# Kernel tuning notes

Measured on AMD Instinct MI355X. Metric: run time of the kernel, lower is better.

## Reference

```python
import jax, jax.numpy as jnp
import numpy as np

N, K, R = 32768, 4096, 256

def setup_inputs() -> dict:
    key = jax.random.key(0)
    k1, k2, k3 = jax.random.split(key, 3)
    H = jax.random.normal(k1, (N, R), dtype=jnp.float32)
    L = jax.random.normal(k2, (K, R), dtype=jnp.float32)
    W_I = jax.random.normal(k3, (R, R), dtype=jnp.float32)
    return {"H": H, "L": L, "W_I": W_I}

def reference(H, L, W_I):
    # Q = W_I @ L^T : (r, k)
    Q = jnp.einsum('rs,ks->rk', W_I, L)
    # M_I = H @ Q : (n, k)
    M_I = jnp.einsum('nr,rk->nk', H, Q)
    A_I = jax.nn.softmax(M_I, axis=1)
    # C_I = A_I @ L : (n, r)
    C_I = jnp.einsum('nk,kr->nr', A_I, L)
    return (C_I, A_I)
```

## Files before the change

kernel.cpp:

```cpp
#include <hip/hip_runtime.h>
#include <hip/hip_bf16.h>
#include <math.h>
#include <stdint.h>

constexpr int N_ROWS = 32768;
constexpr int K_DIM  = 4096;
constexpr int R_DIM  = 256;
constexpr int KP     = 3 * R_DIM;

typedef __bf16 bf16x8 __attribute__((ext_vector_type(8)));
typedef float  f32x4  __attribute__((ext_vector_type(4)));
typedef unsigned short u16x8 __attribute__((ext_vector_type(8)));
typedef unsigned short u16x4 __attribute__((ext_vector_type(4)));

__device__ __forceinline__ unsigned short f2bf(float x) {
    unsigned u = __float_as_uint(x);
    u += 0x7fffu + ((u >> 16) & 1u);
    return (unsigned short)(u >> 16);
}
__device__ __forceinline__ float bf2f(unsigned short h) {
    return __uint_as_float((unsigned)h << 16);
}

__device__ __forceinline__ void gl2lds16(const void* gptr, void* lptr) {
    __builtin_amdgcn_global_load_lds(
        (const __attribute__((address_space(1))) unsigned int*)gptr,
        (__attribute__((address_space(3))) unsigned int*)lptr,
        16, 0, 0);
}

__global__ __launch_bounds__(256)
void gemm_mfma_nt(const unsigned short* __restrict__ A,
                  const unsigned short* __restrict__ B,
                  float* __restrict__ C, int M, int N, int Kc)
{
    __shared__ __align__(16) unsigned short As[128 * 32];
    __shared__ __align__(16) unsigned short Bs[128 * 32];

    const int tid  = threadIdx.x;
    const int wave = tid >> 6, lane = tid & 63;
    const int wm = wave >> 1, wn = wave & 1;
    const long m0 = (long)blockIdx.y * 128;
    const long n0 = (long)blockIdx.x * 128;

    f32x4 acc[4][4] = {};

    const int srow  = lane >> 2;
    const int skoff = (lane & 3) * 8;
    const int c0 = wave, c1 = wave + 4;
    const int kq = (lane >> 4) * 8;
    const int mr = lane & 15;

    for (int k0 = 0; k0 < Kc; k0 += 32) {
        gl2lds16(A + (m0 + c0 * 16 + srow) * (long)Kc + k0 + skoff, &As[c0 * 512]);
        gl2lds16(A + (m0 + c1 * 16 + srow) * (long)Kc + k0 + skoff, &As[c1 * 512]);
        gl2lds16(B + (n0 + c0 * 16 + srow) * (long)Kc + k0 + skoff, &Bs[c0 * 512]);
        gl2lds16(B + (n0 + c1 * 16 + srow) * (long)Kc + k0 + skoff, &Bs[c1 * 512]);
        __syncthreads();

        bf16x8 af[4], bfr[4];
#pragma unroll
        for (int t = 0; t < 4; ++t) {
            af[t]  = *(const bf16x8*)&As[(wm * 64 + t * 16 + mr) * 32 + kq];
            bfr[t] = *(const bf16x8*)&Bs[(wn * 64 + t * 16 + mr) * 32 + kq];
        }
#pragma unroll
        for (int i = 0; i < 4; ++i)
#pragma unroll
            for (int j = 0; j < 4; ++j)
                acc[i][j] = __builtin_amdgcn_mfma_f32_16x16x32_bf16(
                    af[i], bfr[j], acc[i][j], 0, 0, 0);
        __syncthreads();
    }

    const int col = lane & 15, rquad = (lane >> 4) * 4;
#pragma unroll
    for (int i = 0; i < 4; ++i) {
        const long mrow = m0 + wm * 64 + i * 16 + rquad;
#pragma unroll
        for (int j = 0; j < 4; ++j) {
            float* p = C + mrow * (long)N + n0 + wn * 64 + j * 16 + col;
#pragma unroll
            for (int r = 0; r < 4; ++r) p[(long)r * N] = acc[i][j][r];
        }
    }
}

__global__ __launch_bounds__(256)
void k1_ap(const float* __restrict__ A, const float* __restrict__ B,
           unsigned short* __restrict__ Ap)
{
    __shared__ __align__(16) float Asl[16][132];
    __shared__ __align__(16) float Bsl[16][132];
    const int tid = threadIdx.x;
    const int tx = tid & 15, ty = tid >> 4;
    const long m0 = (long)blockIdx.x * 128;
    const long n0 = (long)blockIdx.y * 128;
    const int Kc = R_DIM, N = R_DIM;

    float acc[8][8];
#pragma unroll
    for (int i = 0; i < 8; ++i)
#pragma unroll
        for (int j = 0; j < 8; ++j) acc[i][j] = 0.f;

    for (int k0 = 0; k0 < Kc; k0 += 16) {
#pragma unroll
        for (int q = 0; q < 2; ++q) {
            int fi = tid + 256 * q, row = fi >> 2, col = (fi & 3) * 4;
            float4 v = *(const float4*)(A + (m0 + row) * (long)Kc + k0 + col);
            Asl[col + 0][row] = v.x; Asl[col + 1][row] = v.y;
            Asl[col + 2][row] = v.z; Asl[col + 3][row] = v.w;
        }
#pragma unroll
        for (int q = 0; q < 2; ++q) {
            int fi = tid + 256 * q, row = fi >> 5, col = (fi & 31) * 4;
            float4 v = *(const float4*)(B + (k0 + row) * (long)N + n0 + col);
            *(float4*)&Bsl[row][col] = v;
        }
        __syncthreads();
#pragma unroll
        for (int kk = 0; kk < 16; ++kk) {
            float a[8], b[8];
            *(float4*)&a[0] = *(const float4*)&Asl[kk][ty * 8];
            *(float4*)&a[4] = *(const float4*)&Asl[kk][ty * 8 + 4];
            *(float4*)&b[0] = *(const float4*)&Bsl[kk][tx * 8];
            *(float4*)&b[4] = *(const float4*)&Bsl[kk][tx * 8 + 4];
#pragma unroll
            for (int i = 0; i < 8; ++i)
#pragma unroll
                for (int j = 0; j < 8; ++j)
                    acc[i][j] = fmaf(a[i], b[j], acc[i][j]);
        }
        __syncthreads();
    }
#pragma unroll
    for (int i = 0; i < 8; ++i) {
        const long row = m0 + ty * 8 + i;
        u16x8 hi8, lo8;
#pragma unroll
        for (int j = 0; j < 8; ++j) {
            const unsigned short h = f2bf(acc[i][j]);
            hi8[j] = h;
            lo8[j] = f2bf(acc[i][j] - bf2f(h));
        }
        unsigned short* p = Ap + row * KP + n0 + tx * 8;
        *(u16x8*)(p)              = hi8;
        *(u16x8*)(p + R_DIM)      = hi8;
        *(u16x8*)(p + 2 * R_DIM)  = lo8;
    }
}

__global__ __launch_bounds__(256)
void fused_saw(float* __restrict__ Mio, const unsigned short* __restrict__ LT,
               float* __restrict__ C)
{
    __shared__ __align__(16) unsigned short As[32 * 32];
    __shared__ __align__(16) unsigned short Bs[256 * 32];
    __shared__ float sm[32][8];
    __shared__ float ss[32][8];

    const int tid = threadIdx.x, wave = tid >> 6, lane = tid & 63;
    const long m0 = (long)blockIdx.x * 32;

    const int arow = tid >> 3;
    const int acol = (tid & 7) * 4;
    float* Mrow = Mio + (m0 + arow) * (long)K_DIM;

    {
        float m = -3.4e38f, s = 0.f;
        const float* rp = Mrow + acol;
#pragma unroll 4
        for (int q = 0; q < 128; ++q) {
            float4 v = *(const float4*)(rp + 32 * q);
            float m4 = fmaxf(fmaxf(v.x, v.y), fmaxf(v.z, v.w));
            if (m4 > m) { s *= __expf(m - m4); m = m4; }
            s += __expf(v.x - m) + __expf(v.y - m)
               + __expf(v.z - m) + __expf(v.w - m);
        }
        sm[arow][tid & 7] = m;
        ss[arow][tid & 7] = s;
    }
    __syncthreads();
    float rm, ri;
    {
        float m = sm[arow][0];
#pragma unroll
        for (int t = 1; t < 8; ++t) m = fmaxf(m, sm[arow][t]);
        float S = 0.f;
#pragma unroll
        for (int t = 0; t < 8; ++t) S += ss[arow][t] * __expf(sm[arow][t] - m);
        rm = m; ri = 1.f / S;
    }
    __syncthreads();

    const int srow = lane >> 2, skoff = (lane & 3) * 8;
    const int kq = (lane >> 4) * 8, mr = lane & 15;

    f32x4 acc[2][4] = {};

    for (int k0 = 0; k0 < K_DIM; k0 += 32) {
#pragma unroll
        for (int c4 = 0; c4 < 4; ++c4) {
            const int c = wave * 4 + c4;
            gl2lds16(LT + (c * 16 + srow) * (long)K_DIM + k0 + skoff, &Bs[c * 512]);
        }
        float4 v = *(const float4*)(Mrow + k0 + acol);
        float4 a;
        a.x = __expf(v.x - rm) * ri;
        a.y = __expf(v.y - rm) * ri;
        a.z = __expf(v.z - rm) * ri;
        a.w = __expf(v.w - rm) * ri;
        *(float4*)(Mrow + k0 + acol) = a;
        u16x4 u;
        u[0] = f2bf(a.x); u[1] = f2bf(a.y); u[2] = f2bf(a.z); u[3] = f2bf(a.w);
        *(u16x4*)&As[arow * 32 + acol] = u;
        __syncthreads();

        bf16x8 af[2], bfr[4];
        af[0] = *(const bf16x8*)&As[(mr) * 32 + kq];
        af[1] = *(const bf16x8*)&As[(16 + mr) * 32 + kq];
#pragma unroll
        for (int j = 0; j < 4; ++j)
            bfr[j] = *(const bf16x8*)&Bs[(wave * 64 + j * 16 + mr) * 32 + kq];
#pragma unroll
        for (int i = 0; i < 2; ++i)
#pragma unroll
            for (int j = 0; j < 4; ++j)
                acc[i][j] = __builtin_amdgcn_mfma_f32_16x16x32_bf16(
                    af[i], bfr[j], acc[i][j], 0, 0, 0);
        __syncthreads();
    }

    const int col = lane & 15, rq = (lane >> 4) * 4;
#pragma unroll
    for (int i = 0; i < 2; ++i)
#pragma unroll
        for (int j = 0; j < 4; ++j)
#pragma unroll
            for (int r = 0; r < 4; ++r)
                C[(m0 + i * 16 + rq + r) * (long)R_DIM + wave * 64 + j * 16 + col]
                    = acc[i][j][r];
}

__global__ __launch_bounds__(256)
void prep_B(const float* __restrict__ L, unsigned short* __restrict__ Bp)
{
    const long i = (long)blockIdx.x * 256 + threadIdx.x;
    const long k = i >> 8; const int r = (int)(i & 255);
    const float x = L[i];
    const unsigned short hi = f2bf(x);
    const unsigned short lo = f2bf(x - bf2f(hi));
    unsigned short* row = Bp + k * KP;
    row[r] = hi; row[R_DIM + r] = lo; row[2 * R_DIM + r] = hi;
}

__global__ __launch_bounds__(256)
void prep_LT(const float* __restrict__ L, unsigned short* __restrict__ LT)
{
    const long i = (long)blockIdx.x * 256 + threadIdx.x;
    const long r = i >> 12; const long k = i & 4095;
    LT[r * K_DIM + k] = f2bf(L[k * R_DIM + r]);
}

__global__ __launch_bounds__(256)
void prep_A(const float* __restrict__ P, unsigned short* __restrict__ Ap)
{
    const long i = (long)blockIdx.x * 256 + threadIdx.x;
    const long n = i >> 8; const int r = (int)(i & 255);
    const float x = P[i];
    const unsigned short hi = f2bf(x);
    const unsigned short lo = f2bf(x - bf2f(hi));
    unsigned short* row = Ap + n * KP;
    row[r] = hi; row[R_DIM + r] = hi; row[2 * R_DIM + r] = lo;
}

__global__ __launch_bounds__(256)
void gemm_mfma_a32(const float* __restrict__ A,
                   const unsigned short* __restrict__ B,
                   float* __restrict__ C, int M, int N, int Kc)
{
    __shared__ __align__(16) unsigned short As[128 * 32];
    __shared__ __align__(16) unsigned short Bs[128 * 32];

    const int tid  = threadIdx.x;
    const int wave = tid >> 6, lane = tid & 63;
    const int wm = wave >> 1, wn = wave & 1;
    const long m0 = (long)blockIdx.y * 128;
    const long n0 = (long)blockIdx.x * 128;

    f32x4 acc[4][4] = {};
    const int srow  = lane >> 2, skoff = (lane & 3) * 8;
    const int c0 = wave, c1 = wave + 4;
    const int kq = (lane >> 4) * 8, mr = lane & 15;
    const int arow = tid >> 1, ahalf = (tid & 1) * 16;

    for (int k0 = 0; k0 < Kc; k0 += 32) {
        gl2lds16(B + (n0 + c0 * 16 + srow) * (long)Kc + k0 + skoff, &Bs[c0 * 512]);
        gl2lds16(B + (n0 + c1 * 16 + srow) * (long)Kc + k0 + skoff, &Bs[c1 * 512]);
        {
            const float* g = A + (m0 + arow) * (long)Kc + k0 + ahalf;
            float4 v0 = *(const float4*)(g + 0);
            float4 v1 = *(const float4*)(g + 4);
            float4 v2 = *(const float4*)(g + 8);
            float4 v3 = *(const float4*)(g + 12);
            u16x8 u0, u1;
            u0[0] = f2bf(v0.x); u0[1] = f2bf(v0.y); u0[2] = f2bf(v0.z); u0[3] = f2bf(v0.w);
            u0[4] = f2bf(v1.x); u0[5] = f2bf(v1.y); u0[6] = f2bf(v1.z); u0[7] = f2bf(v1.w);
            u1[0] = f2bf(v2.x); u1[1] = f2bf(v2.y); u1[2] = f2bf(v2.z); u1[3] = f2bf(v2.w);
            u1[4] = f2bf(v3.x); u1[5] = f2bf(v3.y); u1[6] = f2bf(v3.z); u1[7] = f2bf(v3.w);
            *(u16x8*)&As[arow * 32 + ahalf + 0] = u0;
            *(u16x8*)&As[arow * 32 + ahalf + 8] = u1;
        }
        __syncthreads();
        bf16x8 af[4], bfr[4];
#pragma unroll
        for (int t = 0; t < 4; ++t) {
            af[t]  = *(const bf16x8*)&As[(wm * 64 + t * 16 + mr) * 32 + kq];
            bfr[t] = *(const bf16x8*)&Bs[(wn * 64 + t * 16 + mr) * 32 + kq];
        }
#pragma unroll
        for (int i = 0; i < 4; ++i)
#pragma unroll
            for (int j = 0; j < 4; ++j)
                acc[i][j] = __builtin_amdgcn_mfma_f32_16x16x32_bf16(
                    af[i], bfr[j], acc[i][j], 0, 0, 0);
        __syncthreads();
    }
    const int col = lane & 15, rquad = (lane >> 4) * 4;
#pragma unroll
    for (int i = 0; i < 4; ++i) {
        const long mrow = m0 + wm * 64 + i * 16 + rquad;
#pragma unroll
        for (int j = 0; j < 4; ++j) {
            float* p = C + mrow * (long)N + n0 + wn * 64 + j * 16 + col;
#pragma unroll
            for (int r = 0; r < 4; ++r) p[(long)r * N] = acc[i][j][r];
        }
    }
}

template<bool BT>
__global__ __launch_bounds__(256)
void gemm128(const float* __restrict__ A, const float* __restrict__ B,
             float* __restrict__ C, int M, int N, int Kc)
{
    __shared__ __align__(16) float Asl[16][132];
    __shared__ __align__(16) float Bsl[16][132];
    const int tid = threadIdx.x;
    const int tx = tid & 15, ty = tid >> 4;
    const long m0 = (long)blockIdx.x * 128;
    const long n0 = (long)blockIdx.y * 128;
    float acc[8][8];
#pragma unroll
    for (int i = 0; i < 8; ++i)
#pragma unroll
        for (int j = 0; j < 8; ++j) acc[i][j] = 0.f;
    for (int k0 = 0; k0 < Kc; k0 += 16) {
#pragma unroll
        for (int q = 0; q < 2; ++q) {
            int fi = tid + 256 * q, row = fi >> 2, col = (fi & 3) * 4;
            float4 v = *(const float4*)(A + (m0 + row) * (long)Kc + k0 + col);
            Asl[col + 0][row] = v.x; Asl[col + 1][row] = v.y;
            Asl[col + 2][row] = v.z; Asl[col + 3][row] = v.w;
        }
        if (BT) {
#pragma unroll
            for (int q = 0; q < 2; ++q) {
                int fi = tid + 256 * q, row = fi >> 2, col = (fi & 3) * 4;
                float4 v = *(const float4*)(B + (n0 + row) * (long)Kc + k0 + col);
                Bsl[col + 0][row] = v.x; Bsl[col + 1][row] = v.y;
                Bsl[col + 2][row] = v.z; Bsl[col + 3][row] = v.w;
            }
        } else {
#pragma unroll
            for (int q = 0; q < 2; ++q) {
                int fi = tid + 256 * q, row = fi >> 5, col = (fi & 31) * 4;
                float4 v = *(const float4*)(B + (k0 + row) * (long)N + n0 + col);
                *(float4*)&Bsl[row][col] = v;
            }
        }
        __syncthreads();
#pragma unroll
        for (int kk = 0; kk < 16; ++kk) {
            float a[8], b[8];
            *(float4*)&a[0] = *(const float4*)&Asl[kk][ty * 8];
            *(float4*)&a[4] = *(const float4*)&Asl[kk][ty * 8 + 4];
            *(float4*)&b[0] = *(const float4*)&Bsl[kk][tx * 8];
            *(float4*)&b[4] = *(const float4*)&Bsl[kk][tx * 8 + 4];
#pragma unroll
            for (int i = 0; i < 8; ++i)
#pragma unroll
                for (int j = 0; j < 8; ++j)
                    acc[i][j] = fmaf(a[i], b[j], acc[i][j]);
        }
        __syncthreads();
    }
#pragma unroll
    for (int i = 0; i < 8; ++i) {
        float* p = C + (m0 + ty * 8 + i) * (long)N + n0 + tx * 8;
        *(float4*)p       = make_float4(acc[i][0], acc[i][1], acc[i][2], acc[i][3]);
        *(float4*)(p + 4) = make_float4(acc[i][4], acc[i][5], acc[i][6], acc[i][7]);
    }
}

__global__ __launch_bounds__(256)
void softmax_rows(float* __restrict__ Mio)
{
    const long n  = blockIdx.x;
    float* row    = Mio + n * (long)K_DIM;
    const int tid = threadIdx.x;
    float4 v[4];
    float lmax = -3.4e38f;
#pragma unroll
    for (int q = 0; q < 4; ++q) {
        v[q] = ((const float4*)row)[tid + 256 * q];
        lmax = fmaxf(lmax, fmaxf(fmaxf(v[q].x, v[q].y), fmaxf(v[q].z, v[q].w)));
    }
    __shared__ float redmax[4], redsum[4];
#pragma unroll
    for (int off = 32; off > 0; off >>= 1)
        lmax = fmaxf(lmax, __shfl_xor(lmax, off));
    if ((tid & 63) == 0) redmax[tid >> 6] = lmax;
    __syncthreads();
    const float gmax = fmaxf(fmaxf(redmax[0], redmax[1]), fmaxf(redmax[2], redmax[3]));
    float lsum = 0.f;
#pragma unroll
    for (int q = 0; q < 4; ++q) {
        v[q].x = __expf(v[q].x - gmax); v[q].y = __expf(v[q].y - gmax);
        v[q].z = __expf(v[q].z - gmax); v[q].w = __expf(v[q].w - gmax);
        lsum += v[q].x + v[q].y + v[q].z + v[q].w;
    }
#pragma unroll
    for (int off = 32; off > 0; off >>= 1)
        lsum += __shfl_xor(lsum, off);
    if ((tid & 63) == 0) redsum[tid >> 6] = lsum;
    __syncthreads();
    const float inv = 1.f / (redsum[0] + redsum[1] + redsum[2] + redsum[3]);
#pragma unroll
    for (int q = 0; q < 4; ++q) {
        v[q].x *= inv; v[q].y *= inv; v[q].z *= inv; v[q].w *= inv;
        ((float4*)row)[tid + 256 * q] = v[q];
    }
}

extern "C" void kernel_launch(void* const* d_in, const int* in_sizes, int n_in,
                              void* d_out, int out_size, void* d_ws, size_t ws_size,
                              hipStream_t stream)
{
    const float* H  = (const float*)d_in[0];
    const float* L  = (const float*)d_in[1];
    const float* Wi = (const float*)d_in[2];

    float* Cout = (float*)d_out;
    float* Aout = (float*)d_out + (size_t)N_ROWS * R_DIM;

    const size_t szAp = (size_t)N_ROWS * KP * 2;
    const size_t szBp = (size_t)K_DIM * KP * 2;
    const size_t szLT = (size_t)R_DIM * K_DIM * 2;

    if (ws_size >= szAp + szBp + szLT) {
        unsigned short* Ap = (unsigned short*)d_ws;
        unsigned short* Bp = (unsigned short*)((char*)d_ws + szAp);
        unsigned short* LT = (unsigned short*)((char*)d_ws + szAp + szBp);

        k1_ap<<<dim3(N_ROWS / 128, R_DIM / 128), 256, 0, stream>>>(H, Wi, Ap);
        prep_B<<<dim3((K_DIM * R_DIM) / 256), 256, 0, stream>>>(L, Bp);
        prep_LT<<<dim3((R_DIM * K_DIM) / 256), 256, 0, stream>>>(L, LT);
        gemm_mfma_nt<<<dim3(K_DIM / 128, N_ROWS / 128), 256, 0, stream>>>(
            Ap, Bp, Aout, N_ROWS, K_DIM, KP);
        fused_saw<<<dim3(N_ROWS / 32), 256, 0, stream>>>(Aout, LT, Cout);
    } else {
        gemm128<false><<<dim3(N_ROWS / 128, R_DIM / 128), 256, 0, stream>>>(
            H, Wi, Cout, N_ROWS, R_DIM, R_DIM);
        gemm128<true><<<dim3(N_ROWS / 128, K_DIM / 128), 256, 0, stream>>>(
            Cout, L, Aout, N_ROWS, K_DIM, R_DIM);
        softmax_rows<<<dim3(N_ROWS), 256, 0, stream>>>(Aout);
        gemm128<false><<<dim3(N_ROWS / 128, R_DIM / 128), 256, 0, stream>>>(
            Aout, L, Cout, N_ROWS, R_DIM, K_DIM);
    }
}
```

Baseline: 1.345 ms.

## Double-buffer B tiles and build softmax A fragments in registers in fused kernel

```diff
diff --git a/kernel.cpp b/kernel.cpp
--- a/kernel.cpp
+++ b/kernel.cpp
@@ -152,24 +152,22 @@
 }
 
 __global__ __launch_bounds__(256)
-void fused_saw(float* __restrict__ Mio, const unsigned short* __restrict__ LT,
-               float* __restrict__ C)
-{
-    __shared__ __align__(16) unsigned short As[32 * 32];
-    __shared__ __align__(16) unsigned short Bs[256 * 32];
+void fused_saw2(float* __restrict__ Mio, const unsigned short* __restrict__ LT,
+                float* __restrict__ C)
+{
+    __shared__ __align__(16) unsigned short Bs[2][256 * 32];
     __shared__ float sm[32][8];
     __shared__ float ss[32][8];
+    __shared__ float rowm[32];
+    __shared__ float rowiv[32];
 
     const int tid = threadIdx.x, wave = tid >> 6, lane = tid & 63;
     const long m0 = (long)blockIdx.x * 32;
 
-    const int arow = tid >> 3;
-    const int acol = (tid & 7) * 4;
-    float* Mrow = Mio + (m0 + arow) * (long)K_DIM;
-
+    const int arow = tid >> 3, acol = (tid & 7) * 4;
     {
+        const float* rp = Mio + (m0 + arow) * (long)K_DIM + acol;
         float m = -3.4e38f, s = 0.f;
-        const float* rp = Mrow + acol;
 #pragma unroll 4
         for (int q = 0; q < 128; ++q) {
             float4 v = *(const float4*)(rp + 32 * q);
@@ -182,54 +180,93 @@
         ss[arow][tid & 7] = s;
     }
     __syncthreads();
-    float rm, ri;
-    {
+    if ((tid & 7) == 0) {
         float m = sm[arow][0];
 #pragma unroll
         for (int t = 1; t < 8; ++t) m = fmaxf(m, sm[arow][t]);
         float S = 0.f;
 #pragma unroll
         for (int t = 0; t < 8; ++t) S += ss[arow][t] * __expf(sm[arow][t] - m);
-        rm = m; ri = 1.f / S;
-    }
-    __syncthreads();
+        rowm[arow] = m;
+        rowiv[arow] = 1.f / S;
+    }
+    __syncthreads();
+
+    const int fr = lane & 15;
+    const int kq = (lane >> 4) * 8;
+    const float rm0 = rowm[fr],      ri0 = rowiv[fr];
+    const float rm1 = rowm[fr + 16], ri1 = rowiv[fr + 16];
 
     const int srow = lane >> 2, skoff = (lane & 3) * 8;
-    const int kq = (lane >> 4) * 8, mr = lane & 15;
-
-    f32x4 acc[2][4] = {};
-
-    for (int k0 = 0; k0 < K_DIM; k0 += 32) {
+
+    float* R0 = Mio + (m0 + fr) * (long)K_DIM + kq;
+    float* R1 = R0 + 16 * (long)K_DIM;
+
+    auto stageB = [&](int buf, int k0) {
 #pragma unroll
         for (int c4 = 0; c4 < 4; ++c4) {
             const int c = wave * 4 + c4;
-            gl2lds16(LT + (c * 16 + srow) * (long)K_DIM + k0 + skoff, &Bs[c * 512]);
-        }
-        float4 v = *(const float4*)(Mrow + k0 + acol);
-        float4 a;
-        a.x = __expf(v.x - rm) * ri;
-        a.y = __expf(v.y - rm) * ri;
-        a.z = __expf(v.z - rm) * ri;
-        a.w = __expf(v.w - rm) * ri;
-        *(float4*)(Mrow + k0 + acol) = a;
-        u16x4 u;
-        u[0] = f2bf(a.x); u[1] = f2bf(a.y); u[2] = f2bf(a.z); u[3] = f2bf(a.w);
-        *(u16x4*)&As[arow * 32 + acol] = u;
-        __syncthreads();
-
-        bf16x8 af[2], bfr[4];
-        af[0] = *(const bf16x8*)&As[(mr) * 32 + kq];
-        af[1] = *(const bf16x8*)&As[(16 + mr) * 32 + kq];
+            gl2lds16(LT + (c * 16 + srow) * (long)K_DIM + k0 + skoff,
+                     &Bs[buf][c * 512]);
+        }
+    };
+
+    f32x4 acc[2][4] = {};
+    float4 va00, va01, va10, va11;
+    float4 vn00 = {}, vn01 = {}, vn10 = {}, vn11 = {};
+
+    constexpr int NIT = K_DIM / 32;
+    int cb = 0;
+    stageB(0, 0);
+    va00 = *(const float4*)(R0);     va01 = *(const float4*)(R0 + 4);
+    va10 = *(const float4*)(R1);     va11 = *(const float4*)(R1 + 4);
+    __syncthreads();
+
+#pragma unroll 1
+    for (int it = 0; it < NIT; ++it) {
+        const int k0 = it * 32;
+        if (it + 1 < NIT) {
+            stageB(cb ^ 1, k0 + 32);
+            vn00 = *(const float4*)(R0 + k0 + 32);
+            vn01 = *(const float4*)(R0 + k0 + 36);
+            vn10 = *(const float4*)(R1 + k0 + 32);
+            vn11 = *(const float4*)(R1 + k0 + 36);
+        }
+
+        float x0[8] = {va00.x, va00.y, va00.z, va00.w,
+                       va01.x, va01.y, va01.z, va01.w};
+        float x1[8] = {va10.x, va10.y, va10.z, va10.w,
+                       va11.x, va11.y, va11.z, va11.w};
+        float e0[8], e1[8];
+        u16x8 p0, p1;
+#pragma unroll
+        for (int j = 0; j < 8; ++j) {
+            e0[j] = __expf(x0[j] - rm0) * ri0;  p0[j] = f2bf(e0[j]);
+            e1[j] = __expf(x1[j] - rm1) * ri1;  p1[j] = f2bf(e1[j]);
+        }
+        if (wave == 0) {
+            *(float4*)(R0 + k0)     = make_float4(e0[0], e0[1], e0[2], e0[3]);
+            *(float4*)(R0 + k0 + 4) = make_float4(e0[4], e0[5], e0[6], e0[7]);
+            *(float4*)(R1 + k0)     = make_float4(e1[0], e1[1], e1[2], e1[3]);
+            *(float4*)(R1 + k0 + 4) = make_float4(e1[4], e1[5], e1[6], e1[7]);
+        }
+
+        const bf16x8 af0 = __builtin_bit_cast(bf16x8, p0);
+        const bf16x8 af1 = __builtin_bit_cast(bf16x8, p1);
+        bf16x8 bfr[4];
 #pragma unroll
         for (int j = 0; j < 4; ++j)
-            bfr[j] = *(const bf16x8*)&Bs[(wave * 64 + j * 16 + mr) * 32 + kq];
-#pragma unroll
-        for (int i = 0; i < 2; ++i)
-#pragma unroll
-            for (int j = 0; j < 4; ++j)
-                acc[i][j] = __builtin_amdgcn_mfma_f32_16x16x32_bf16(
-                    af[i], bfr[j], acc[i][j], 0, 0, 0);
-        __syncthreads();
+            bfr[j] = *(const bf16x8*)&Bs[cb][(wave * 64 + j * 16 + fr) * 32 + kq];
+#pragma unroll
+        for (int j = 0; j < 4; ++j) {
+            acc[0][j] = __builtin_amdgcn_mfma_f32_16x16x32_bf16(
+                af0, bfr[j], acc[0][j], 0, 0, 0);
+            acc[1][j] = __builtin_amdgcn_mfma_f32_16x16x32_bf16(
+                af1, bfr[j], acc[1][j], 0, 0, 0);
+        }
+        __syncthreads();
+        cb ^= 1;
+        va00 = vn00; va01 = vn01; va10 = vn10; va11 = vn11;
     }
 
     const int col = lane & 15, rq = (lane >> 4) * 4;
@@ -258,85 +295,22 @@
 __global__ __launch_bounds__(256)
 void prep_LT(const float* __restrict__ L, unsigned short* __restrict__ LT)
 {
-    const long i = (long)blockIdx.x * 256 + threadIdx.x;
-    const long r = i >> 12; const long k = i & 4095;
-    LT[r * K_DIM + k] = f2bf(L[k * R_DIM + r]);
-}
-
-__global__ __launch_bounds__(256)
-void prep_A(const float* __restrict__ P, unsigned short* __restrict__ Ap)
-{
-    const long i = (long)blockIdx.x * 256 + threadIdx.x;
-    const long n = i >> 8; const int r = (int)(i & 255);
-    const float x = P[i];
-    const unsigned short hi = f2bf(x);
-    const unsigned short lo = f2bf(x - bf2f(hi));
-    unsigned short* row = Ap + n * KP;
-    row[r] = hi; row[R_DIM + r] = hi; row[2 * R_DIM + r] = lo;
-}
-
-__global__ __launch_bounds__(256)
-void gemm_mfma_a32(const float* __restrict__ A,
-                   const unsigned short* __restrict__ B,
-                   float* __restrict__ C, int M, int N, int Kc)
-{
-    __shared__ __align__(16) unsigned short As[128 * 32];
-    __shared__ __align__(16) unsigned short Bs[128 * 32];
-
-    const int tid  = threadIdx.x;
-    const int wave = tid >> 6, lane = tid & 63;
-    const int wm = wave >> 1, wn = wave & 1;
-    const long m0 = (long)blockIdx.y * 128;
-    const long n0 = (long)blockIdx.x * 128;
-
-    f32x4 acc[4][4] = {};
-    const int srow  = lane >> 2, skoff = (lane & 3) * 8;
-    const int c0 = wave, c1 = wave + 4;
-    const int kq = (lane >> 4) * 8, mr = lane & 15;
-    const int arow = tid >> 1, ahalf = (tid & 1) * 16;
-
-    for (int k0 = 0; k0 < Kc; k0 += 32) {
-        gl2lds16(B + (n0 + c0 * 16 + srow) * (long)Kc + k0 + skoff, &Bs[c0 * 512]);
-        gl2lds16(B + (n0 + c1 * 16 + srow) * (long)Kc + k0 + skoff, &Bs[c1 * 512]);
-        {
-            const float* g = A + (m0 + arow) * (long)Kc + k0 + ahalf;
-            float4 v0 = *(const float4*)(g + 0);
-            float4 v1 = *(const float4*)(g + 4);
-            float4 v2 = *(const float4*)(g + 8);
-            float4 v3 = *(const float4*)(g + 12);
-            u16x8 u0, u1;
-            u0[0] = f2bf(v0.x); u0[1] = f2bf(v0.y); u0[2] = f2bf(v0.z); u0[3] = f2bf(v0.w);
-            u0[4] = f2bf(v1.x); u0[5] = f2bf(v1.y); u0[6] = f2bf(v1.z); u0[7] = f2bf(v1.w);
-            u1[0] = f2bf(v2.x); u1[1] = f2bf(v2.y); u1[2] = f2bf(v2.z); u1[3] = f2bf(v2.w);
-            u1[4] = f2bf(v3.x); u1[5] = f2bf(v3.y); u1[6] = f2bf(v3.z); u1[7] = f2bf(v3.w);
-            *(u16x8*)&As[arow * 32 + ahalf + 0] = u0;
-            *(u16x8*)&As[arow * 32 + ahalf + 8] = u1;
-        }
-        __syncthreads();
-        bf16x8 af[4], bfr[4];
-#pragma unroll
-        for (int t = 0; t < 4; ++t) {
-            af[t]  = *(const bf16x8*)&As[(wm * 64 + t * 16 + mr) * 32 + kq];
-            bfr[t] = *(const bf16x8*)&Bs[(wn * 64 + t * 16 + mr) * 32 + kq];
-        }
-#pragma unroll
-        for (int i = 0; i < 4; ++i)
-#pragma unroll
-            for (int j = 0; j < 4; ++j)
-                acc[i][j] = __builtin_amdgcn_mfma_f32_16x16x32_bf16(
-                    af[i], bfr[j], acc[i][j], 0, 0, 0);
-        __syncthreads();
-    }
-    const int col = lane & 15, rquad = (lane >> 4) * 4;
-#pragma unroll
-    for (int i = 0; i < 4; ++i) {
-        const long mrow = m0 + wm * 64 + i * 16 + rquad;
-#pragma unroll
-        for (int j = 0; j < 4; ++j) {
-            float* p = C + mrow * (long)N + n0 + wn * 64 + j * 16 + col;
-#pragma unroll
-            for (int r = 0; r < 4; ++r) p[(long)r * N] = acc[i][j][r];
-        }
+    __shared__ unsigned short t[64][66];
+    const int k0 = blockIdx.x * 64;
+    const int r0 = blockIdx.y * 64;
+    const int tid = threadIdx.x;
+#pragma unroll
+    for (int q = 0; q < 16; ++q) {
+        const int e = q * 256 + tid;
+        const int kk = e >> 6, rr = e & 63;
+        t[rr][kk] = f2bf(L[(long)(k0 + kk) * R_DIM + r0 + rr]);
+    }
+    __syncthreads();
+#pragma unroll
+    for (int q = 0; q < 16; ++q) {
+        const int e = q * 256 + tid;
+        const int rr = e >> 6, kk = e & 63;
+        LT[(long)(r0 + rr) * K_DIM + k0 + kk] = t[rr][kk];
     }
 }
 
@@ -466,10 +440,10 @@
 
         k1_ap<<<dim3(N_ROWS / 128, R_DIM / 128), 256, 0, stream>>>(H, Wi, Ap);
         prep_B<<<dim3((K_DIM * R_DIM) / 256), 256, 0, stream>>>(L, Bp);
-        prep_LT<<<dim3((R_DIM * K_DIM) / 256), 256, 0, stream>>>(L, LT);
+        prep_LT<<<dim3(K_DIM / 64, R_DIM / 64), 256, 0, stream>>>(L, LT);
         gemm_mfma_nt<<<dim3(K_DIM / 128, N_ROWS / 128), 256, 0, stream>>>(
             Ap, Bp, Aout, N_ROWS, K_DIM, KP);
-        fused_saw<<<dim3(N_ROWS / 32), 256, 0, stream>>>(Aout, LT, Cout);
+        fused_saw2<<<dim3(N_ROWS / 32), 256, 0, stream>>>(Aout, LT, Cout);
     } else {
         gemm128<false><<<dim3(N_ROWS / 128, R_DIM / 128), 256, 0, stream>>>(
             H, Wi, Cout, N_ROWS, R_DIM, R_DIM);
```

Result: slower. 1.490 ms (+10.8%).
